# Performance work log

Measured on AMD Instinct MI355X. Metric: run time of the kernel, lower is better.

The kernel has to match this reference:

```python
import jax, jax.numpy as jnp
import numpy as np

N, E, G = 50000, 800000, 64
IN_NODE, OUT_NODE, IN_EDGE = 16, 20, 16
HID_E, N_ACT, HID_C = 64, 8, 256
BN_EPS = 1e-5


def setup_inputs() -> dict:
    key = jax.random.key(0)
    ks = jax.random.split(key, 12)
    def w(i, shape, scale=0.05):
        return jax.random.normal(ks[i], shape, jnp.float32) * scale
    return {
        "x": jax.random.normal(ks[0], (N, IN_NODE), jnp.float32),
        "edge_attr": jax.random.normal(ks[1], (E, IN_EDGE), jnp.float32),
        "a": jax.random.normal(ks[2], (G, N_ACT), jnp.float32),
        "edge_index": jax.random.randint(ks[3], (2, E), 0, N),
        "batch": jnp.sort(jax.random.randint(ks[4], (N,), 0, G)),
        # edge-conditioning MLP: Lin(16,64) -> BN(64) -> ReLU -> Lin(64, 16*20)
        "W1": w(5, (IN_EDGE, HID_E)), "b1": jnp.zeros((HID_E,), jnp.float32),
        "gamma": jnp.ones((HID_E,), jnp.float32), "beta": jnp.zeros((HID_E,), jnp.float32),
        "W2": w(6, (HID_E, IN_NODE * OUT_NODE)), "b2": jnp.zeros((IN_NODE * OUT_NODE,), jnp.float32),
        # NNConv root weight + bias
        "root_w": w(7, (IN_NODE, OUT_NODE)), "bias": jnp.zeros((OUT_NODE,), jnp.float32),
        # critic head: Lin(20+8,256) -> ReLU -> Lin(256,1)
        "Wc1": w(8, (OUT_NODE + N_ACT, HID_C)), "bc1": jnp.zeros((HID_C,), jnp.float32),
        "Wc2": w(9, (HID_C, 1)), "bc2": jnp.zeros((1,), jnp.float32),
    }


def reference(x, edge_attr, a, W1, b1, gamma, beta, W2, b2, root_w, bias,
              Wc1, bc1, Wc2, bc2, edge_index, batch):
    # edge-conditioning MLP (BatchNorm in training mode: batch stats over edges)
    h = edge_attr @ W1 + b1                              # [E, 64]
    mu = jnp.mean(h, axis=0)
    var = jnp.mean(jnp.square(h - mu), axis=0)           # biased var, as BN fwd
    h = (h - mu) * jax.lax.rsqrt(var + BN_EPS) * gamma + beta
    h = jax.nn.relu(h)
    w_e = (h @ W2 + b2).reshape(E, IN_NODE, OUT_NODE)    # per-edge weight matrix

    src, dst = edge_index[0], edge_index[1]
    msg = jnp.einsum('ei,eio->eo', x[src], w_e)          # gather + per-edge matvec [E, 20]
    aggr = jax.ops.segment_sum(msg, dst, num_segments=N) # scatter-add (NNConv aggr='add')
    out = x @ root_w + aggr + bias                       # [N, 20]

    # global mean pool over graphs
    sums = jax.ops.segment_sum(out, batch, num_segments=G)            # [G, 20]
    cnt = jax.ops.segment_sum(jnp.ones((N, 1), out.dtype), batch, num_segments=G)
    pooled = sums / jnp.maximum(cnt, 1.0)

    z = jnp.concatenate([pooled, a], axis=1)             # [G, 28]
    z = jax.nn.relu(z @ Wc1 + bc1)
    return z @ Wc2 + bc2                                 # [G, 1]
```

## Files before the change

kernel.cpp:

```cpp
#include <hip/hip_runtime.h>


#define E_EDGES   800000
#define N_NODES   50000
#define G_GRAPHS  64
#define EDGE_GRID 6144
#define NGROUPS   50000
#define GSTRIDE   1536
#define NSUP      256
#define STAT_GRID 512
#define QSCALE    131072.0f
#define QINV      (1.0f / 131072.0f)

typedef _Float16 f16x2 __attribute__((ext_vector_type(2)));
typedef _Float16 f16x8 __attribute__((ext_vector_type(8)));
typedef __fp16   fp16x2 __attribute__((ext_vector_type(2)));
typedef float    f32x4 __attribute__((ext_vector_type(4)));
typedef unsigned u32x4 __attribute__((ext_vector_type(4)));

union H2U { f16x2 h; unsigned u; };
union F8U { f16x8 v; f16x2 h2[4]; u32x4 u4; };

__device__ __forceinline__ f16x2 pkrtz(float a, float b) {
  fp16x2 r = __builtin_amdgcn_cvt_pkrtz(a, b);
  return __builtin_bit_cast(f16x2, r);
}

__device__ __forceinline__ int q17(float x) {
  float r = __builtin_fmaf(x, QSCALE, 12582912.0f);
  return __builtin_bit_cast(int, r) - 0x4B400000;
}

__global__ __launch_bounds__(256) void setup_kernel(
    const float* __restrict__ W2, const float* __restrict__ b2,
    const float* __restrict__ W1, const float* __restrict__ x,
    const float* __restrict__ ea, unsigned* __restrict__ Bbuf,
    unsigned* __restrict__ Bw1, unsigned* __restrict__ xh,
    float* __restrict__ gstatsT)
{
  __shared__ float red[4][272];
  const int b = blockIdx.x, tid = threadIdx.x;
  if (b < STAT_GRID) {
    int lane = tid & 63, wave = tid >> 6;
    int nl = lane & 15, q = lane >> 4;
    int gw = b * 4 + wave;
    f32x4 acc = (f32x4){0.f, 0.f, 0.f, 0.f};
    float ms = 0.f;
    for (int c0 = gw; c0 < E_EDGES / 32; c0 += STAT_GRID * 4) {
      const float* p = ea + (size_t)(c0 * 32 + q * 8) * 16 + nl;
      float v0 = p[0],  v1 = p[16], v2 = p[32], v3 = p[48];
      float v4 = p[64], v5 = p[80], v6 = p[96], v7 = p[112];
      ms += (v0 + v1) + (v2 + v3) + (v4 + v5) + (v6 + v7);
      F8U av;
      av.h2[0] = pkrtz(v0, v1); av.h2[1] = pkrtz(v2, v3);
      av.h2[2] = pkrtz(v4, v5); av.h2[3] = pkrtz(v6, v7);
      acc = __builtin_amdgcn_mfma_f32_16x16x32_f16(av.v, av.v, acc, 0, 0, 0);
    }
    ms += __shfl_xor(ms, 16, 64);
    ms += __shfl_xor(ms, 32, 64);
#pragma unroll
    for (int r = 0; r < 4; ++r) red[wave][(q * 4 + r) * 16 + nl] = acc[r];
    if (q == 0) red[wave][256 + nl] = ms;
    __syncthreads();
    for (int v = tid; v < 272; v += 256)
      gstatsT[(size_t)v * STAT_GRID + b] =
          red[0][v] + red[1][v] + red[2][v] + red[3][v];
  } else if (b < STAT_GRID + 70) {
    int idx = (b - STAT_GRID) * 256 + tid;
    if (idx < 33 * 512) {
      int r = idx & 3, lane = (idx >> 2) & 63, nt = (idx >> 8) & 1,
          s = idx >> 9;
      int q = lane >> 4, nl = lane & 15, n = nt * 16 + nl;
      float v0 = 0.f, v1 = 0.f;
      if (n < 20) {
        if (s < 32) {
          int K0 = s * 32 + q * 8 + 2 * r;
          v0 = W2[(K0 >> 4) * 320 + (K0 & 15) * 20 + n];
          v1 = W2[((K0 + 1) >> 4) * 320 + ((K0 + 1) & 15) * 20 + n];
        } else if (q < 2) {
          int i0 = q * 8 + 2 * r;
          v0 = b2[i0 * 20 + n];
          v1 = b2[(i0 + 1) * 20 + n];
        }
      }
      H2U pk; pk.h = pkrtz(v0, v1);
      Bbuf[idx] = pk.u;
    } else {
      int idx2 = idx - 33 * 512;
      int r = idx2 & 3, lane = (idx2 >> 2) & 63, nt = idx2 >> 8;
      int q = lane >> 4, nl = lane & 15, n = nt * 16 + nl;
      int k0 = q * 8 + 2 * r;
      float v0 = (k0 < 16)     ? W1[k0 * 64 + n]       : 0.f;
      float v1 = (k0 + 1 < 16) ? W1[(k0 + 1) * 64 + n] : 0.f;
      H2U pk; pk.h = pkrtz(v0, v1);
      Bw1[idx2] = pk.u;
    }
  } else {
    int i = (b - STAT_GRID - 70) * 256 + tid;
    if (i < N_NODES * 8) {
      H2U pk; pk.h = pkrtz(x[2 * i], x[2 * i + 1]);
      xh[i] = pk.u;
    }
  }
}

__global__ __launch_bounds__(256) void mid_kernel(
    const float* __restrict__ gstatsT, const float* __restrict__ W1,
    const float* __restrict__ b1, const float* __restrict__ gamma,
    const float* __restrict__ beta, const float* __restrict__ x,
    const int* __restrict__ batch, float* __restrict__ sc,
    float* __restrict__ sh, float* __restrict__ sumx,
    float* __restrict__ cntf)
{
  const int t = threadIdx.x;
  if (blockIdx.x == G_GRAPHS) {
    __shared__ float S[272];
    for (int v = t; v < 272; v += 256) {
      const float* p = gstatsT + (size_t)v * STAT_GRID;
      float s0 = 0.f, s1 = 0.f, s2 = 0.f, s3 = 0.f;
      for (int bb = 0; bb < STAT_GRID; bb += 4) {
        s0 += p[bb]; s1 += p[bb + 1]; s2 += p[bb + 2]; s3 += p[bb + 3];
      }
      S[v] = (s0 + s1) + (s2 + s3);
    }
    __syncthreads();
    if (t < 64) {
      float w[16];
#pragma unroll
      for (int j = 0; j < 16; ++j) w[j] = W1[j * 64 + t];
      const float invE = 1.0f / (float)E_EDGES;
      float mw = 0.f;
#pragma unroll
      for (int j = 0; j < 16; ++j) mw += S[256 + j] * w[j];
      mw *= invE;
      float qf = 0.f;
      for (int j = 0; j < 16; ++j) {
        float tt = 0.f;
#pragma unroll
        for (int j2 = 0; j2 < 16; ++j2) tt += S[j * 16 + j2] * w[j2];
        qf += w[j] * tt;
      }
      qf *= invE;
      float b = b1[t];
      float meanH = mw + b;
      float eh2 = qf + 2.f * b * mw + b * b;
      float var = eh2 - meanH * meanH;
      float s = gamma[t] * rsqrtf(var + 1e-5f);
      sc[t] = s;
      sh[t] = beta[t] + (b - meanH) * s;
    }
  } else {
    int g = blockIdx.x;
    __shared__ int se[2];
    if (t < 2) {
      int key = g + t;
      int lo = 0, hi = N_NODES;
      while (lo < hi) {
        int mid = (lo + hi) >> 1;
        if (batch[mid] < key) lo = mid + 1; else hi = mid;
      }
      se[t] = lo;
    }
    __syncthreads();
    int start = se[0], end = se[1];
    int c = t & 15, rr = t >> 4;
    float s = 0.f;
    for (int n = start + rr; n < end; n += 16) s += x[(size_t)n * 16 + c];
    __shared__ float red[256];
    red[t] = s;
    __syncthreads();
#pragma unroll
    for (int st = 128; st >= 16; st >>= 1) {
      if (t < st) red[t] += red[t + st];
      __syncthreads();
    }
    if (t < 16) sumx[g * 16 + t] = red[t];
    if (t == 0) cntf[g] = (float)(end - start);
  }
}

__global__ __launch_bounds__(64, 3) void edge_kernel(
    const unsigned* __restrict__ xh, const float* __restrict__ ea,
    const int* __restrict__ ei, const int* __restrict__ batch,
    const float* __restrict__ sc, const float* __restrict__ sh,
    const unsigned* __restrict__ Bbuf, const unsigned* __restrict__ Bw1v,
    int* __restrict__ gpartI)
{
  __shared__ unsigned hh[640];
  __shared__ int gacc[1280];
  const int lane = threadIdx.x;
  const int nl = lane & 15, q = lane >> 4;
  const int s = blockIdx.x;
  const int kq = (s >> 3) & 3;
  const int sgroup = ((s >> 5) << 3) | (s & 7);
  const int* srcp = ei;
  const int* dstp = ei + E_EDGES;

  for (int v = lane; v < 1280; v += 64) gacc[v] = 0;

  F8U bb[8][2];
#pragma unroll
  for (int sl = 0; sl < 8; ++sl)
#pragma unroll
    for (int nt = 0; nt < 2; ++nt)
      bb[sl][nt].u4 =
          ((const u32x4*)Bbuf)[((kq * 8 + sl) * 2 + nt) * 64 + lane];
  F8U bx[2];
  if (kq == 3) {
    bx[0].u4 = ((const u32x4*)Bbuf)[64 * 64 + lane];
    bx[1].u4 = ((const u32x4*)Bbuf)[65 * 64 + lane];
  } else {
    bx[0].u4 = (u32x4){0u, 0u, 0u, 0u};
    bx[1].u4 = (u32x4){0u, 0u, 0u, 0u};
  }
  F8U bw1; bw1.u4 = ((const u32x4*)Bw1v)[kq * 64 + lane];
  const float scv = sc[kq * 16 + nl];
  const float shv = sh[kq * 16 + nl];
  const int hrb = (q >> 1) * 20 + nl;
  const int qh = q & 1;

  int g = sgroup;
  u32x4 xp  = (u32x4){0u,0u,0u,0u};
  int   ge20 = 0;
  f32x4 eaAn = (f32x4){0.f,0.f,0.f,0.f}, eaBn = eaAn;
  int   srcn = 0, dstn = 0;
  f32x4 eaA2 = eaAn, eaB2 = eaAn;
  int   src2 = 0, dst2 = 0;
  u32x4 xpn = xp;
  int   gen20 = 0;

  {
    int base = g * 16 + nl;
    int src0 = srcp[base];
    int dst0 = dstp[base];
    xp = ((const u32x4*)xh)[src0 * 2 + qh];
    ge20 = batch[dst0] * 20;
    f32x4 eaA0 = (f32x4){0.f,0.f,0.f,0.f}, eaB0 = eaA0;
    if (q < 2) {
      const float* p = ea + (size_t)base * 16 + q * 8;
      eaA0 = *(const f32x4*)p;
      eaB0 = *(const f32x4*)(p + 4);
    }
    F8U aEA;
    if (q < 2) {
      aEA.h2[0] = pkrtz(eaA0[0], eaA0[1]); aEA.h2[1] = pkrtz(eaA0[2], eaA0[3]);
      aEA.h2[2] = pkrtz(eaB0[0], eaB0[1]); aEA.h2[3] = pkrtz(eaB0[2], eaB0[3]);
    } else {
      aEA.u4 = (u32x4){0u, 0u, 0u, 0u};
    }
    f32x4 hD = __builtin_amdgcn_mfma_f32_16x16x32_f16(
        aEA.v, bw1.v, (f32x4){0.f, 0.f, 0.f, 0.f}, 0, 0, 0);
#pragma unroll
    for (int r = 0; r < 4; ++r) {
      float h = fmaxf(hD[r] * scv + shv, 0.f);
      H2U pk; pk.h = pkrtz(h, h);
      hh[nl * 20 + q * 4 + r] = pk.u;
    }
  }
  if (g + GSTRIDE < NGROUPS) {
    int base = (g + GSTRIDE) * 16 + nl;
    srcn = srcp[base];
    dstn = dstp[base];
    if (q < 2) {
      const float* p = ea + (size_t)base * 16 + q * 8;
      eaAn = *(const f32x4*)p;
      eaBn = *(const f32x4*)(p + 4);
    }
  }
  int cur = 0;

  while (g < NGROUPS) {
    const int gn = g + GSTRIDE, gnn = gn + GSTRIDE;
    const bool hvalid = (gn < NGROUPS);

    if (gnn < NGROUPS) {
      int base = gnn * 16 + nl;
      src2 = srcp[base];
      dst2 = dstp[base];
      if (q < 2) {
        const float* p = ea + (size_t)base * 16 + q * 8;
        eaA2 = *(const f32x4*)p;
        eaB2 = *(const f32x4*)(p + 4);
      }
    }
    if (hvalid) {
      xpn = ((const u32x4*)xh)[srcn * 2 + qh];
      gen20 = batch[dstn] * 20;
    }

    unsigned hu[8];
#pragma unroll
    for (int sl = 0; sl < 8; ++sl) hu[sl] = hh[cur * 320 + hrb + sl * 40];
    const int gq0 = __shfl(ge20, q * 4 + 0, 64);
    const int gq1 = __shfl(ge20, q * 4 + 1, 64);
    const int gq2 = __shfl(ge20, q * 4 + 2, 64);
    const int gq3 = __shfl(ge20, q * 4 + 3, 64);

    f32x4 hDn = (f32x4){0.f, 0.f, 0.f, 0.f};
    if (hvalid) {
      F8U aEA;
      if (q < 2) {
        aEA.h2[0] = pkrtz(eaAn[0], eaAn[1]);
        aEA.h2[1] = pkrtz(eaAn[2], eaAn[3]);
        aEA.h2[2] = pkrtz(eaBn[0], eaBn[1]);
        aEA.h2[3] = pkrtz(eaBn[2], eaBn[3]);
      } else {
        aEA.u4 = (u32x4){0u, 0u, 0u, 0u};
      }
      hDn = __builtin_amdgcn_mfma_f32_16x16x32_f16(
          aEA.v, bw1.v, (f32x4){0.f, 0.f, 0.f, 0.f}, 0, 0, 0);
    }

    F8U xcur; xcur.u4 = xp;
    f32x4 a00 = (f32x4){0.f, 0.f, 0.f, 0.f};
    f32x4 a01 = a00, a10 = a00, a11 = a00;
#pragma unroll
    for (int sl = 0; sl < 8; sl += 2) {
      H2U u0; u0.u = hu[sl];
      H2U u1; u1.u = hu[sl + 1];
      F8U av0, av1;
      av0.h2[0] = u0.h * xcur.h2[0];
      av0.h2[1] = u0.h * xcur.h2[1];
      av0.h2[2] = u0.h * xcur.h2[2];
      av0.h2[3] = u0.h * xcur.h2[3];
      av1.h2[0] = u1.h * xcur.h2[0];
      av1.h2[1] = u1.h * xcur.h2[1];
      av1.h2[2] = u1.h * xcur.h2[2];
      av1.h2[3] = u1.h * xcur.h2[3];
      a00 = __builtin_amdgcn_mfma_f32_16x16x32_f16(av0.v, bb[sl][0].v, a00,
                                                   0, 0, 0);
      a10 = __builtin_amdgcn_mfma_f32_16x16x32_f16(av0.v, bb[sl][1].v, a10,
                                                   0, 0, 0);
      a01 = __builtin_amdgcn_mfma_f32_16x16x32_f16(av1.v, bb[sl + 1][0].v,
                                                   a01, 0, 0, 0);
      a11 = __builtin_amdgcn_mfma_f32_16x16x32_f16(av1.v, bb[sl + 1][1].v,
                                                   a11, 0, 0, 0);
    }
    if (kq == 3) {
      F8U av;
      if (q < 2) av = xcur;
      else       av.u4 = (u32x4){0u, 0u, 0u, 0u};
      a00 = __builtin_amdgcn_mfma_f32_16x16x32_f16(av.v, bx[0].v, a00,
                                                   0, 0, 0);
      a10 = __builtin_amdgcn_mfma_f32_16x16x32_f16(av.v, bx[1].v, a10,
                                                   0, 0, 0);
    }
    const f32x4 acc0 = a00 + a01;
    const f32x4 acc1 = a10 + a11;

    if (hvalid) {
      const int hw = (cur ^ 1) * 320 + nl * 20 + q * 4;
#pragma unroll
      for (int r = 0; r < 4; ++r) {
        float h = fmaxf(hDn[r] * scv + shv, 0.f);
        H2U pk; pk.h = pkrtz(h, h);
        hh[hw + r] = pk.u;
      }
    }

    {
      atomicAdd(&gacc[gq0 + nl], q17(acc0[0]));
      if (nl < 4) atomicAdd(&gacc[gq0 + 16 + nl], q17(acc1[0]));
      atomicAdd(&gacc[gq1 + nl], q17(acc0[1]));
      if (nl < 4) atomicAdd(&gacc[gq1 + 16 + nl], q17(acc1[1]));
      atomicAdd(&gacc[gq2 + nl], q17(acc0[2]));
      if (nl < 4) atomicAdd(&gacc[gq2 + 16 + nl], q17(acc1[2]));
      atomicAdd(&gacc[gq3 + nl], q17(acc0[3]));
      if (nl < 4) atomicAdd(&gacc[gq3 + 16 + nl], q17(acc1[3]));
    }

    g = gn; cur ^= 1;
    xp = xpn; ge20 = gen20;
    srcn = src2; dstn = dst2;
    eaAn = eaA2; eaBn = eaB2;
  }

  const int ssup = s & (NSUP - 1);
  for (int v = lane; v < 1280; v += 64) {
    int gg = v / 20, o = v - gg * 20;
    atomicAdd(&gpartI[(gg * NSUP + ssup) * 20 + o], gacc[v]);
  }
}

__global__ __launch_bounds__(256) void critic_kernel(
    const int* __restrict__ gpartI, const float* __restrict__ sumx,
    const float* __restrict__ cntf, const float* __restrict__ root_w,
    const float* __restrict__ bias, const float* __restrict__ a,
    const float* __restrict__ Wc1, const float* __restrict__ bc1,
    const float* __restrict__ Wc2, const float* __restrict__ bc2,
    float* __restrict__ out)
{
  int g = blockIdx.x, t = threadIdx.x;
  __shared__ int part[240];
  __shared__ float pooled[20];
  if (t < 240) {
    int col = t % 20, r = t / 20;
    int s = 0;
    const int* gp = gpartI + (size_t)g * NSUP * 20;
    for (int sl = r; sl < NSUP; sl += 12) s += gp[sl * 20 + col];
    part[t] = s;
  }
  __syncthreads();
  if (t < 20) {
    int si = 0;
#pragma unroll
    for (int r = 0; r < 12; ++r) si += part[r * 20 + t];
    float s = (float)si * QINV;
    float cnt = cntf[g];
    float base = bias[t] * cnt;
#pragma unroll
    for (int i = 0; i < 16; ++i) base += sumx[g * 16 + i] * root_w[i * 20 + t];
    pooled[t] = (s + base) / fmaxf(cnt, 1.f);
  }
  __syncthreads();
  float z = bc1[t];
#pragma unroll
  for (int j = 0; j < 20; ++j) z += pooled[j] * Wc1[j * 256 + t];
#pragma unroll
  for (int j = 0; j < 8; ++j) z += a[g * 8 + j] * Wc1[(20 + j) * 256 + t];
  z = fmaxf(z, 0.f);
  float pr = z * Wc2[t];
#pragma unroll
  for (int off = 32; off >= 1; off >>= 1) pr += __shfl_down(pr, off, 64);
  __shared__ float red[4];
  if ((t & 63) == 0) red[t >> 6] = pr;
  __syncthreads();
  if (t == 0) out[g] = red[0] + red[1] + red[2] + red[3] + bc2[0];
}

extern "C" void kernel_launch(void* const* d_in, const int* in_sizes, int n_in,
                              void* d_out, int out_size, void* d_ws,
                              size_t ws_size, hipStream_t stream) {
  const float* x         = (const float*)d_in[0];
  const float* edge_attr = (const float*)d_in[1];
  const float* a         = (const float*)d_in[2];
  const int*   ei        = (const int*)d_in[3];
  const int*   batch     = (const int*)d_in[4];
  const float* W1        = (const float*)d_in[5];
  const float* b1        = (const float*)d_in[6];
  const float* gamma     = (const float*)d_in[7];
  const float* beta      = (const float*)d_in[8];
  const float* W2        = (const float*)d_in[9];
  const float* b2        = (const float*)d_in[10];
  const float* root_w    = (const float*)d_in[11];
  const float* bias      = (const float*)d_in[12];
  const float* Wc1       = (const float*)d_in[13];
  const float* bc1       = (const float*)d_in[14];
  const float* Wc2       = (const float*)d_in[15];
  const float* bc2       = (const float*)d_in[16];
  float* out = (float*)d_out;

  float* wsf     = (float*)d_ws;
  float* sc      = wsf;
  float* sh      = wsf + 64;
  float* sumx    = wsf + 128;
  float* cntf    = wsf + 1152;
  unsigned* Bw1  = (unsigned*)(wsf + 1216);
  unsigned* Bbuf = (unsigned*)(wsf + 2240);
  float* gstatsT = wsf + 19136;
  unsigned* xhp  = (unsigned*)(wsf + 158400);
  int* gpartI    = (int*)(wsf + 558400);

  (void)hipMemsetAsync(gpartI, 0, (size_t)G_GRAPHS * NSUP * 20 * sizeof(int),
                       stream);

  const int XCONV_BLOCKS = (N_NODES * 8 + 255) / 256;
  setup_kernel<<<STAT_GRID + 70 + XCONV_BLOCKS, 256, 0, stream>>>(
      W2, b2, W1, x, edge_attr, Bbuf, Bw1, xhp, gstatsT);
  mid_kernel<<<G_GRAPHS + 1, 256, 0, stream>>>(gstatsT, W1, b1, gamma, beta,
                                               x, batch, sc, sh, sumx, cntf);
  edge_kernel<<<EDGE_GRID, 64, 0, stream>>>(xhp, edge_attr, ei, batch, sc,
                                            sh, Bbuf, Bw1, gpartI);
  critic_kernel<<<G_GRAPHS, 256, 0, stream>>>(gpartI, sumx, cntf, root_w,
                                              bias, a, Wc1, bc1, Wc2, bc2,
                                              out);
}
```

Baseline: 242.0 us.

## Merge four K-quarter wavefronts into one block sharing staged edge data

Each edge group used to be processed by four separate 64-thread blocks, one per K quarter, and each block loaded the same source rows, batch ids and edge attributes itself. Now a 256-thread block holds all four K quarters as waves. Waves 0, 1 and 2 take turns prefetching the shared x rows, graph ids and edge attributes into double-buffered LDS, and all four waves read from there. This removes the duplicated global loads and the shuffles, at the cost of a block-wide barrier every iteration and more LDS per block.

```diff
diff --git a/kernel.cpp b/kernel.cpp
--- a/kernel.cpp
+++ b/kernel.cpp
@@ -4,9 +4,9 @@
 #define E_EDGES   800000
 #define N_NODES   50000
 #define G_GRAPHS  64
-#define EDGE_GRID 6144
+#define EDGE_GRID 3072
 #define NGROUPS   50000
-#define GSTRIDE   1536
+#define GSTRIDE   3072
 #define NSUP      256
 #define STAT_GRID 512
 #define QSCALE    131072.0f
@@ -179,24 +179,28 @@
   }
 }
 
-__global__ __launch_bounds__(64, 3) void edge_kernel(
+__global__ __launch_bounds__(256, 4) void edge_kernel(
     const unsigned* __restrict__ xh, const float* __restrict__ ea,
     const int* __restrict__ ei, const int* __restrict__ batch,
     const float* __restrict__ sc, const float* __restrict__ sh,
     const unsigned* __restrict__ Bbuf, const unsigned* __restrict__ Bw1v,
     int* __restrict__ gpartI)
 {
-  __shared__ unsigned hh[640];
+  __shared__ unsigned hh[4][640];
   __shared__ int gacc[1280];
-  const int lane = threadIdx.x;
+  __shared__ float sEA[2][256];
+  __shared__ unsigned sXH[2][128];
+  __shared__ int sGE[2][16];
+  __shared__ unsigned sBX[2][256];
+
+  const int tid = threadIdx.x;
+  const int w = tid >> 6;
+  const int lane = tid & 63;
   const int nl = lane & 15, q = lane >> 4;
-  const int s = blockIdx.x;
-  const int kq = (s >> 3) & 3;
-  const int sgroup = ((s >> 5) << 3) | (s & 7);
-  const int* srcp = ei;
-  const int* dstp = ei + E_EDGES;
-
-  for (int v = lane; v < 1280; v += 64) gacc[v] = 0;
+  const int qh = q & 1;
+  const int kq = w;
+
+  for (int v = tid; v < 1280; v += 256) gacc[v] = 0;
 
   F8U bb[8][2];
 #pragma unroll
@@ -205,105 +209,111 @@
     for (int nt = 0; nt < 2; ++nt)
       bb[sl][nt].u4 =
           ((const u32x4*)Bbuf)[((kq * 8 + sl) * 2 + nt) * 64 + lane];
-  F8U bx[2];
-  if (kq == 3) {
-    bx[0].u4 = ((const u32x4*)Bbuf)[64 * 64 + lane];
-    bx[1].u4 = ((const u32x4*)Bbuf)[65 * 64 + lane];
-  } else {
-    bx[0].u4 = (u32x4){0u, 0u, 0u, 0u};
-    bx[1].u4 = (u32x4){0u, 0u, 0u, 0u};
-  }
   F8U bw1; bw1.u4 = ((const u32x4*)Bw1v)[kq * 64 + lane];
   const float scv = sc[kq * 16 + nl];
   const float shv = sh[kq * 16 + nl];
   const int hrb = (q >> 1) * 20 + nl;
-  const int qh = q & 1;
-
-  int g = sgroup;
-  u32x4 xp  = (u32x4){0u,0u,0u,0u};
-  int   ge20 = 0;
-  f32x4 eaAn = (f32x4){0.f,0.f,0.f,0.f}, eaBn = eaAn;
-  int   srcn = 0, dstn = 0;
-  f32x4 eaA2 = eaAn, eaB2 = eaAn;
-  int   src2 = 0, dst2 = 0;
-  u32x4 xpn = xp;
-  int   gen20 = 0;
+
+  if (w == 3) {
+    u32x4 b0 = ((const u32x4*)Bbuf)[64 * 64 + lane];
+    u32x4 b1 = ((const u32x4*)Bbuf)[65 * 64 + lane];
+    *(u32x4*)&sBX[0][lane * 4] = b0;
+    *(u32x4*)&sBX[1][lane * 4] = b1;
+  }
+
+  const int* srcp = ei;
+  const int* dstp = ei + E_EDGES;
+  int g = blockIdx.x;
+  const int g1 = g + GSTRIDE;
+  int srcg = 0, dstg = 0;
 
   {
-    int base = g * 16 + nl;
-    int src0 = srcp[base];
-    int dst0 = dstp[base];
-    xp = ((const u32x4*)xh)[src0 * 2 + qh];
-    ge20 = batch[dst0] * 20;
-    f32x4 eaA0 = (f32x4){0.f,0.f,0.f,0.f}, eaB0 = eaA0;
+    const int base0 = g * 16;
+    f32x4 eA = (f32x4){0.f, 0.f, 0.f, 0.f}, eB = eA;
     if (q < 2) {
-      const float* p = ea + (size_t)base * 16 + q * 8;
-      eaA0 = *(const f32x4*)p;
-      eaB0 = *(const f32x4*)(p + 4);
+      const float* p = ea + (size_t)(base0 + nl) * 16 + q * 8;
+      eA = *(const f32x4*)p;
+      eB = *(const f32x4*)(p + 4);
     }
     F8U aEA;
     if (q < 2) {
-      aEA.h2[0] = pkrtz(eaA0[0], eaA0[1]); aEA.h2[1] = pkrtz(eaA0[2], eaA0[3]);
-      aEA.h2[2] = pkrtz(eaB0[0], eaB0[1]); aEA.h2[3] = pkrtz(eaB0[2], eaB0[3]);
+      aEA.h2[0] = pkrtz(eA[0], eA[1]); aEA.h2[1] = pkrtz(eA[2], eA[3]);
+      aEA.h2[2] = pkrtz(eB[0], eB[1]); aEA.h2[3] = pkrtz(eB[2], eB[3]);
     } else {
       aEA.u4 = (u32x4){0u, 0u, 0u, 0u};
     }
     f32x4 hD = __builtin_amdgcn_mfma_f32_16x16x32_f16(
         aEA.v, bw1.v, (f32x4){0.f, 0.f, 0.f, 0.f}, 0, 0, 0);
+    u32x4 hwv;
 #pragma unroll
     for (int r = 0; r < 4; ++r) {
       float h = fmaxf(hD[r] * scv + shv, 0.f);
       H2U pk; pk.h = pkrtz(h, h);
-      hh[nl * 20 + q * 4 + r] = pk.u;
-    }
-  }
-  if (g + GSTRIDE < NGROUPS) {
-    int base = (g + GSTRIDE) * 16 + nl;
-    srcn = srcp[base];
-    dstn = dstp[base];
-    if (q < 2) {
-      const float* p = ea + (size_t)base * 16 + q * 8;
-      eaAn = *(const f32x4*)p;
-      eaBn = *(const f32x4*)(p + 4);
-    }
-  }
+      hwv[r] = pk.u;
+    }
+    *(u32x4*)&hh[w][nl * 20 + q * 4] = hwv;
+
+    if (w == 0) {
+      if (lane < 32) {
+        int s0 = srcp[base0 + (lane >> 1)];
+        u32x4 xv = ((const u32x4*)xh)[s0 * 2 + (lane & 1)];
+        *(u32x4*)&sXH[0][lane * 4] = xv;
+        srcg = srcp[g1 * 16 + (lane >> 1)];
+      }
+    } else if (w == 2) {
+      if (lane < 16) {
+        int d0 = dstp[base0 + lane];
+        sGE[0][lane] = batch[d0];
+        dstg = dstp[g1 * 16 + lane];
+      }
+    } else if (w == 1) {
+      f32x4 ev = *(const f32x4*)(ea + (size_t)g1 * 256 + lane * 4);
+      *(f32x4*)&sEA[0][lane * 4] = ev;
+    }
+  }
+  __syncthreads();
+
   int cur = 0;
-
   while (g < NGROUPS) {
-    const int gn = g + GSTRIDE, gnn = gn + GSTRIDE;
-    const bool hvalid = (gn < NGROUPS);
-
-    if (gnn < NGROUPS) {
-      int base = gnn * 16 + nl;
-      src2 = srcp[base];
-      dst2 = dstp[base];
-      if (q < 2) {
-        const float* p = ea + (size_t)base * 16 + q * 8;
-        eaA2 = *(const f32x4*)p;
-        eaB2 = *(const f32x4*)(p + 4);
-      }
-    }
-    if (hvalid) {
-      xpn = ((const u32x4*)xh)[srcn * 2 + qh];
-      gen20 = batch[dstn] * 20;
-    }
-
+    const int gn = g + GSTRIDE, g2 = gn + GSTRIDE;
+    const bool hv = (gn < NGROUPS);
+
+    u32x4 xstg;
+    f32x4 estg;
+    int gestg = 0, src2 = 0, dst2 = 0;
+    if (w == 0) {
+      if (lane < 32) {
+        if (hv) xstg = ((const u32x4*)xh)[srcg * 2 + (lane & 1)];
+        if (g2 < NGROUPS) src2 = srcp[g2 * 16 + (lane >> 1)];
+      }
+    } else if (w == 2) {
+      if (lane < 16) {
+        if (hv) gestg = batch[dstg];
+        if (g2 < NGROUPS) dst2 = dstp[g2 * 16 + lane];
+      }
+    } else if (w == 1) {
+      if (g2 < NGROUPS)
+        estg = *(const f32x4*)(ea + (size_t)g2 * 256 + lane * 4);
+    }
+
+    F8U xcur;
+    xcur.u4 = *(const u32x4*)&sXH[cur][(nl * 2 + qh) * 4];
+    const int ge0 = sGE[cur][q * 4 + 0] * 20;
+    const int ge1 = sGE[cur][q * 4 + 1] * 20;
+    const int ge2v = sGE[cur][q * 4 + 2] * 20;
+    const int ge3 = sGE[cur][q * 4 + 3] * 20;
     unsigned hu[8];
 #pragma unroll
-    for (int sl = 0; sl < 8; ++sl) hu[sl] = hh[cur * 320 + hrb + sl * 40];
-    const int gq0 = __shfl(ge20, q * 4 + 0, 64);
-    const int gq1 = __shfl(ge20, q * 4 + 1, 64);
-    const int gq2 = __shfl(ge20, q * 4 + 2, 64);
-    const int gq3 = __shfl(ge20, q * 4 + 3, 64);
+    for (int sl = 0; sl < 8; ++sl) hu[sl] = hh[w][cur * 320 + hrb + sl * 40];
 
     f32x4 hDn = (f32x4){0.f, 0.f, 0.f, 0.f};
-    if (hvalid) {
+    if (hv) {
       F8U aEA;
       if (q < 2) {
-        aEA.h2[0] = pkrtz(eaAn[0], eaAn[1]);
-        aEA.h2[1] = pkrtz(eaAn[2], eaAn[3]);
-        aEA.h2[2] = pkrtz(eaBn[0], eaBn[1]);
-        aEA.h2[3] = pkrtz(eaBn[2], eaBn[3]);
+        f32x4 eA = *(const f32x4*)&sEA[cur][nl * 16 + q * 8];
+        f32x4 eB = *(const f32x4*)&sEA[cur][nl * 16 + q * 8 + 4];
+        aEA.h2[0] = pkrtz(eA[0], eA[1]); aEA.h2[1] = pkrtz(eA[2], eA[3]);
+        aEA.h2[2] = pkrtz(eB[0], eB[1]); aEA.h2[3] = pkrtz(eB[2], eB[3]);
       } else {
         aEA.u4 = (u32x4){0u, 0u, 0u, 0u};
       }
@@ -311,7 +321,6 @@
           aEA.v, bw1.v, (f32x4){0.f, 0.f, 0.f, 0.f}, 0, 0, 0);
     }
 
-    F8U xcur; xcur.u4 = xp;
     f32x4 a00 = (f32x4){0.f, 0.f, 0.f, 0.f};
     f32x4 a01 = a00, a10 = a00, a11 = a00;
 #pragma unroll
@@ -337,46 +346,56 @@
                                                    a11, 0, 0, 0);
     }
     if (kq == 3) {
+      F8U bxa, bxb;
+      bxa.u4 = *(const u32x4*)&sBX[0][lane * 4];
+      bxb.u4 = *(const u32x4*)&sBX[1][lane * 4];
       F8U av;
       if (q < 2) av = xcur;
       else       av.u4 = (u32x4){0u, 0u, 0u, 0u};
-      a00 = __builtin_amdgcn_mfma_f32_16x16x32_f16(av.v, bx[0].v, a00,
+      a00 = __builtin_amdgcn_mfma_f32_16x16x32_f16(av.v, bxa.v, a00,
                                                    0, 0, 0);
-      a10 = __builtin_amdgcn_mfma_f32_16x16x32_f16(av.v, bx[1].v, a10,
+      a10 = __builtin_amdgcn_mfma_f32_16x16x32_f16(av.v, bxb.v, a10,
                                                    0, 0, 0);
     }
     const f32x4 acc0 = a00 + a01;
     const f32x4 acc1 = a10 + a11;
 
-    if (hvalid) {
-      const int hw = (cur ^ 1) * 320 + nl * 20 + q * 4;
+    if (hv) {
+      u32x4 hwv;
 #pragma unroll
       for (int r = 0; r < 4; ++r) {
         float h = fmaxf(hDn[r] * scv + shv, 0.f);
         H2U pk; pk.h = pkrtz(h, h);
-        hh[hw + r] = pk.u;
-      }
+        hwv[r] = pk.u;
+      }
+      *(u32x4*)&hh[w][(cur ^ 1) * 320 + nl * 20 + q * 4] = hwv;
+    }
+    if (w == 0) {
+      if (lane < 32 && hv) *(u32x4*)&sXH[cur ^ 1][lane * 4] = xstg;
+    } else if (w == 2) {
+      if (lane < 16 && hv) sGE[cur ^ 1][lane] = gestg;
+    } else if (w == 1) {
+      if (g2 < NGROUPS) *(f32x4*)&sEA[cur ^ 1][lane * 4] = estg;
     }
 
     {
-      atomicAdd(&gacc[gq0 + nl], q17(acc0[0]));
-      if (nl < 4) atomicAdd(&gacc[gq0 + 16 + nl], q17(acc1[0]));
-      atomicAdd(&gacc[gq1 + nl], q17(acc0[1]));
-      if (nl < 4) atomicAdd(&gacc[gq1 + 16 + nl], q17(acc1[1]));
-      atomicAdd(&gacc[gq2 + nl], q17(acc0[2]));
-      if (nl < 4) atomicAdd(&gacc[gq2 + 16 + nl], q17(acc1[2]));
-      atomicAdd(&gacc[gq3 + nl], q17(acc0[3]));
-      if (nl < 4) atomicAdd(&gacc[gq3 + 16 + nl], q17(acc1[3]));
-    }
-
+      atomicAdd(&gacc[ge0 + nl], q17(acc0[0]));
+      if (nl < 4) atomicAdd(&gacc[ge0 + 16 + nl], q17(acc1[0]));
+      atomicAdd(&gacc[ge1 + nl], q17(acc0[1]));
+      if (nl < 4) atomicAdd(&gacc[ge1 + 16 + nl], q17(acc1[1]));
+      atomicAdd(&gacc[ge2v + nl], q17(acc0[2]));
+      if (nl < 4) atomicAdd(&gacc[ge2v + 16 + nl], q17(acc1[2]));
+      atomicAdd(&gacc[ge3 + nl], q17(acc0[3]));
+      if (nl < 4) atomicAdd(&gacc[ge3 + 16 + nl], q17(acc1[3]));
+    }
+
+    __syncthreads();
     g = gn; cur ^= 1;
-    xp = xpn; ge20 = gen20;
-    srcn = src2; dstn = dst2;
-    eaAn = eaA2; eaBn = eaB2;
-  }
-
-  const int ssup = s & (NSUP - 1);
-  for (int v = lane; v < 1280; v += 64) {
+    srcg = src2; dstg = dst2;
+  }
+
+  const int ssup = blockIdx.x & (NSUP - 1);
+  for (int v = tid; v < 1280; v += 256) {
     int gg = v / 20, o = v - gg * 20;
     atomicAdd(&gpartI[(gg * NSUP + ssup) * 20 + o], gacc[v]);
   }
@@ -469,8 +488,8 @@
       W2, b2, W1, x, edge_attr, Bbuf, Bw1, xhp, gstatsT);
   mid_kernel<<<G_GRAPHS + 1, 256, 0, stream>>>(gstatsT, W1, b1, gamma, beta,
                                                x, batch, sc, sh, sumx, cntf);
-  edge_kernel<<<EDGE_GRID, 64, 0, stream>>>(xhp, edge_attr, ei, batch, sc,
-                                            sh, Bbuf, Bw1, gpartI);
+  edge_kernel<<<EDGE_GRID, 256, 0, stream>>>(xhp, edge_attr, ei, batch, sc,
+                                             sh, Bbuf, Bw1, gpartI);
   critic_kernel<<<G_GRAPHS, 256, 0, stream>>>(gpartI, sumx, cntf, root_w,
                                               bias, a, Wc1, bc1, Wc2, bc2,
                                               out);
```

Result: slower. 292.4 us (+20.9%).
